# Optimization experiments

Hardware: AMD Instinct MI355X
Metric: run time of the kernel (lower is better)

Reference implementation:

```python
import jax, jax.numpy as jnp
import numpy as np

D_MODEL = 1024
N_HEADS = 16
HEAD_DIM = D_MODEL // N_HEADS
KV_LATENT = 512
N_EXPERTS = 4
D_HIDDEN = 4 * D_MODEL
B, T = 2, 1024


def rmsnorm(x, w, eps=1e-6):
    return w * (x * jax.lax.rsqrt(jnp.mean(x * x, axis=-1, keepdims=True) + eps))


def layernorm(x, g, b, eps=1e-5):
    mu = jnp.mean(x, axis=-1, keepdims=True)
    var = jnp.mean((x - mu) ** 2, axis=-1, keepdims=True)
    return (x - mu) * jax.lax.rsqrt(var + eps) * g + b


def apply_rope(x):
    # x: [b, h, t, d], half-split RoPE as in the torch source
    t, d = x.shape[2], x.shape[3]
    half = d // 2
    pos = jnp.arange(t, dtype=x.dtype)[:, None]                      # [t,1]
    inv_freq = 1.0 / (10000.0 ** (jnp.arange(half, dtype=x.dtype) / half))
    ang = pos * inv_freq[None, :]                                    # [t,half]
    sin, cos = jnp.sin(ang), jnp.cos(ang)
    x1, x2 = x[..., :half], x[..., half:]
    return jnp.concatenate([x1 * cos - x2 * sin, x1 * sin + x2 * cos], axis=-1)


def setup_inputs() -> dict:
    key = jax.random.key(0)
    ks = jax.random.split(key, 16)
    s = lambda fan_in: 1.0 / np.sqrt(fan_in)
    return {
        "x": jax.random.normal(ks[0], (B, T, D_MODEL), jnp.float32),
        "norm1_w": jnp.ones((D_MODEL,), jnp.float32),
        "norm2_w": jnp.ones((D_MODEL,), jnp.float32),
        "Wq": jax.random.normal(ks[1], (D_MODEL, D_MODEL), jnp.float32) * s(D_MODEL),
        "Wdkv": jax.random.normal(ks[2], (KV_LATENT, D_MODEL), jnp.float32) * s(D_MODEL),
        "Wuk": jax.random.normal(ks[3], (D_MODEL, KV_LATENT), jnp.float32) * s(KV_LATENT),
        "Wuv": jax.random.normal(ks[4], (D_MODEL, KV_LATENT), jnp.float32) * s(KV_LATENT),
        "Wo": jax.random.normal(ks[5], (D_MODEL, D_MODEL), jnp.float32) * s(D_MODEL),
        "ln_g": jnp.ones((KV_LATENT,), jnp.float32),
        "ln_b": jnp.zeros((KV_LATENT,), jnp.float32),
        "gate_w": jax.random.normal(ks[6], (N_EXPERTS, D_MODEL), jnp.float32) * s(D_MODEL),
        "gate_b": jnp.zeros((N_EXPERTS,), jnp.float32),
        "W1": jax.random.normal(ks[7], (N_EXPERTS, D_HIDDEN, D_MODEL), jnp.float32) * s(D_MODEL),
        "b1": jnp.zeros((N_EXPERTS, D_HIDDEN), jnp.float32),
        "W2": jax.random.normal(ks[8], (N_EXPERTS, D_MODEL, D_HIDDEN), jnp.float32) * s(D_HIDDEN),
        "b2": jnp.zeros((N_EXPERTS, D_MODEL), jnp.float32),
    }


def mla_attention(x, Wq, Wdkv, Wuk, Wuv, Wo, ln_g, ln_b):
    b, t, _ = x.shape
    q = (x @ Wq.T).reshape(b, t, N_HEADS, HEAD_DIM).transpose(0, 2, 1, 3)  # [b,h,t,dh]
    latent = layernorm(x @ Wdkv.T, ln_g, ln_b)                             # [b,t,L]
    k = (latent @ Wuk.T).reshape(b, t, N_HEADS, HEAD_DIM).transpose(0, 2, 1, 3)
    v = (latent @ Wuv.T).reshape(b, t, N_HEADS, HEAD_DIM).transpose(0, 2, 1, 3)
    q = apply_rope(q)
    k = apply_rope(k)
    scores = jnp.einsum("bhqd,bhkd->bhqk", q, k) / np.sqrt(HEAD_DIM)
    causal = jnp.tril(jnp.ones((t, t), dtype=bool))
    scores = jnp.where(causal, scores, -jnp.inf)
    attn = jax.nn.softmax(scores, axis=-1)  # dropout is identity in eval
    out = jnp.einsum("bhqk,bhkd->bhqd", attn, v).transpose(0, 2, 1, 3).reshape(b, t, D_MODEL)
    return out @ Wo.T


def moe(x, gate_w, gate_b, W1, b1, W2, b2):
    # top-1 routing: each token goes to exactly one expert (argmax of gate)
    logits = x @ gate_w.T + gate_b                                  # [b,t,E]
    top = jnp.argmax(logits, axis=-1)                               # [b,t]
    onehot = jax.nn.one_hot(top, N_EXPERTS, dtype=x.dtype)          # [b,t,E]
    h = jax.nn.relu(jnp.einsum("btd,ehd->bteh", x, W1) + b1)        # [b,t,E,H]
    y = jnp.einsum("bteh,edh->bted", h, W2) + b2                    # [b,t,E,D]
    return jnp.einsum("bted,bte->btd", y, onehot)


def reference(x, norm1_w, norm2_w, Wq, Wdkv, Wuk, Wuv, Wo, ln_g, ln_b,
              gate_w, gate_b, W1, b1, W2, b2):
    x = x + mla_attention(rmsnorm(x, norm1_w), Wq, Wdkv, Wuk, Wuv, Wo, ln_g, ln_b)
    x = x + moe(rmsnorm(x, norm2_w), gate_w, gate_b, W1, b1, W2, b2)
    return x
```

## Files before the change

### kernel.cpp

```cpp
#include <hip/hip_runtime.h>
#include <hip/hip_bf16.h>
#include <math.h>

typedef unsigned short u16;
typedef __attribute__((ext_vector_type(4))) float floatx4;
typedef __attribute__((ext_vector_type(8))) short shortx8;

#define DEVI static __device__ __forceinline__

DEVI u16 f2b(float f) {
  union { float f; unsigned int i; } v; v.f = f;
  unsigned int x = v.i;
  return (u16)((x + 0x7fffu + ((x >> 16) & 1u)) >> 16);
}

constexpr int T_ = 1024, D_ = 1024, HD_ = 64, KV_ = 512, DH_ = 4096, M_ = 2048;
#define NEGBIG (-1e30f)

__global__ __launch_bounds__(256) void k_rms1b(const float* __restrict__ x, const float* __restrict__ w,
                                               u16* __restrict__ outb) {
  int row = blockIdx.x, tid = threadIdx.x;
  float4 v = *(const float4*)&x[(size_t)row * D_ + tid * 4];
  float ss = v.x*v.x + v.y*v.y + v.z*v.z + v.w*v.w;
  #pragma unroll
  for (int m = 32; m >= 1; m >>= 1) ss += __shfl_xor(ss, m, 64);
  __shared__ float red[4];
  if ((tid & 63) == 0) red[tid >> 6] = ss;
  __syncthreads();
  ss = red[0] + red[1] + red[2] + red[3];
  float sc = 1.0f / sqrtf(ss * (1.0f / 1024.0f) + 1e-6f);
  float4 wv = *(const float4*)&w[tid * 4];
  ushort4 ob;
  ob.x = f2b(wv.x*v.x*sc); ob.y = f2b(wv.y*v.y*sc);
  ob.z = f2b(wv.z*v.z*sc); ob.w = f2b(wv.w*v.w*sc);
  *(ushort4*)&outb[(size_t)row * D_ + tid * 4] = ob;
}

__global__ __launch_bounds__(256) void k_rms2b(const float* __restrict__ x, const float* __restrict__ w,
                                               float* __restrict__ outf, u16* __restrict__ outb) {
  int row = blockIdx.x, tid = threadIdx.x;
  float4 v = *(const float4*)&x[(size_t)row * D_ + tid * 4];
  float ss = v.x*v.x + v.y*v.y + v.z*v.z + v.w*v.w;
  #pragma unroll
  for (int m = 32; m >= 1; m >>= 1) ss += __shfl_xor(ss, m, 64);
  __shared__ float red[4];
  if ((tid & 63) == 0) red[tid >> 6] = ss;
  __syncthreads();
  ss = red[0] + red[1] + red[2] + red[3];
  float sc = 1.0f / sqrtf(ss * (1.0f / 1024.0f) + 1e-6f);
  float4 wv = *(const float4*)&w[tid * 4];
  float4 o; o.x = wv.x*v.x*sc; o.y = wv.y*v.y*sc; o.z = wv.z*v.z*sc; o.w = wv.w*v.w*sc;
  *(float4*)&outf[(size_t)row * D_ + tid * 4] = o;
  ushort4 ob; ob.x = f2b(o.x); ob.y = f2b(o.y); ob.z = f2b(o.z); ob.w = f2b(o.w);
  *(ushort4*)&outb[(size_t)row * D_ + tid * 4] = ob;
}

__global__ __launch_bounds__(256) void k_lnb(const float* __restrict__ lat, const float* __restrict__ g,
                                             const float* __restrict__ bb, u16* __restrict__ ob) {
  int row = blockIdx.x, tid = threadIdx.x;
  const float* r = lat + (size_t)row * KV_;
  float v0 = r[tid], v1 = r[tid + 256];
  float s = v0 + v1;
  #pragma unroll
  for (int m = 32; m >= 1; m >>= 1) s += __shfl_xor(s, m, 64);
  __shared__ float red[4];
  if ((tid & 63) == 0) red[tid >> 6] = s;
  __syncthreads();
  float mu = (red[0] + red[1] + red[2] + red[3]) * (1.0f / 512.0f);
  __syncthreads();
  float d0 = v0 - mu, d1 = v1 - mu;
  float ss = d0*d0 + d1*d1;
  #pragma unroll
  for (int m = 32; m >= 1; m >>= 1) ss += __shfl_xor(ss, m, 64);
  if ((tid & 63) == 0) red[tid >> 6] = ss;
  __syncthreads();
  float var = (red[0] + red[1] + red[2] + red[3]) * (1.0f / 512.0f);
  float sc = 1.0f / sqrtf(var + 1e-5f);
  ob[(size_t)row * KV_ + tid]       = f2b(d0 * sc * g[tid]       + bb[tid]);
  ob[(size_t)row * KV_ + tid + 256] = f2b(d1 * sc * g[tid + 256] + bb[tid + 256]);
}

__global__ __launch_bounds__(256) void k_cvtall(const float* __restrict__ W1, const float* __restrict__ W2,
                                                const float* __restrict__ Wq, const float* __restrict__ Wdkv,
                                                const float* __restrict__ Wuk, const float* __restrict__ Wuv,
                                                const float* __restrict__ Wo, u16* __restrict__ dst) {
  for (size_t i = (size_t)blockIdx.x * 256 + threadIdx.x; i < 9306112ull; i += (size_t)gridDim.x * 256) {
    const float* s;
    if      (i < 4194304ull) s = W1   + i * 4;
    else if (i < 8388608ull) s = W2   + (i - 4194304ull) * 4;
    else if (i < 8650752ull) s = Wq   + (i - 8388608ull) * 4;
    else if (i < 8781824ull) s = Wdkv + (i - 8650752ull) * 4;
    else if (i < 8912896ull) s = Wuk  + (i - 8781824ull) * 4;
    else if (i < 9043968ull) s = Wuv  + (i - 8912896ull) * 4;
    else                     s = Wo   + (i - 9043968ull) * 4;
    float4 f = *(const float4*)s;
    ushort4 u; u.x = f2b(f.x); u.y = f2b(f.y); u.z = f2b(f.z); u.w = f2b(f.w);
    *(ushort4*)(dst + i * 4) = u;
  }
}

template<int BF16B>
__global__ __launch_bounds__(256) void k_gemm_t(const u16* __restrict__ A, const void* __restrict__ Bp,
                                                const float* __restrict__ resid, float* __restrict__ Cf,
                                                u16* __restrict__ Cb, int N, int K) {
  int bid = blockIdx.x;
  int xcd = bid & 7, jj = bid >> 3;
  int mt = jj & 31, nt = (jj >> 5) * 8 + xcd;
  __shared__ __align__(16) u16 As[64][72];
  __shared__ __align__(16) u16 Bs[64][72];
  int tid = threadIdx.x, lane = tid & 63, wave = tid >> 6;
  int wm = (wave >> 1) * 32, wn = (wave & 1) * 32;
  int lr = tid >> 2, lc = (tid & 3) * 16;
  const u16* arow = A + (size_t)(mt * 64 + lr) * K + lc;
  const u16* browb = (const u16*)Bp + (size_t)(nt * 64 + lr) * K + lc;
  const float* browf = (const float*)Bp + (size_t)(nt * 64 + lr) * K + lc;
  floatx4 z = {0.f, 0.f, 0.f, 0.f};
  floatx4 acc00 = z, acc01 = z, acc10 = z, acc11 = z;
  int fm = lane & 15, fkq = (lane >> 4) * 8;
  uint4 ra0 = *(const uint4*)&arow[0];
  uint4 ra1 = *(const uint4*)&arow[8];
  uint4 rbA, rbB; float4 rb0, rb1, rb2, rb3;
  if constexpr (BF16B) {
    rbA = *(const uint4*)&browb[0]; rbB = *(const uint4*)&browb[8];
  } else {
    rb0 = *(const float4*)&browf[0];  rb1 = *(const float4*)&browf[4];
    rb2 = *(const float4*)&browf[8];  rb3 = *(const float4*)&browf[12];
  }
  for (int kb = 0; kb < K; kb += 64) {
    *(uint4*)&As[lr][lc]     = ra0;
    *(uint4*)&As[lr][lc + 8] = ra1;
    if constexpr (BF16B) {
      *(uint4*)&Bs[lr][lc]     = rbA;
      *(uint4*)&Bs[lr][lc + 8] = rbB;
    } else {
      ushort4 u;
      u.x = f2b(rb0.x); u.y = f2b(rb0.y); u.z = f2b(rb0.z); u.w = f2b(rb0.w); *(ushort4*)&Bs[lr][lc]      = u;
      u.x = f2b(rb1.x); u.y = f2b(rb1.y); u.z = f2b(rb1.z); u.w = f2b(rb1.w); *(ushort4*)&Bs[lr][lc + 4]  = u;
      u.x = f2b(rb2.x); u.y = f2b(rb2.y); u.z = f2b(rb2.z); u.w = f2b(rb2.w); *(ushort4*)&Bs[lr][lc + 8]  = u;
      u.x = f2b(rb3.x); u.y = f2b(rb3.y); u.z = f2b(rb3.z); u.w = f2b(rb3.w); *(ushort4*)&Bs[lr][lc + 12] = u;
    }
    __syncthreads();
    if (kb + 64 < K) {
      ra0 = *(const uint4*)&arow[kb + 64];
      ra1 = *(const uint4*)&arow[kb + 72];
      if constexpr (BF16B) {
        rbA = *(const uint4*)&browb[kb + 64]; rbB = *(const uint4*)&browb[kb + 72];
      } else {
        rb0 = *(const float4*)&browf[kb + 64]; rb1 = *(const float4*)&browf[kb + 68];
        rb2 = *(const float4*)&browf[kb + 72]; rb3 = *(const float4*)&browf[kb + 76];
      }
    }
    #pragma unroll
    for (int ks = 0; ks < 64; ks += 32) {
      shortx8 a0  = *(const shortx8*)&As[wm + fm][ks + fkq];
      shortx8 a1  = *(const shortx8*)&As[wm + 16 + fm][ks + fkq];
      shortx8 b0  = *(const shortx8*)&Bs[wn + fm][ks + fkq];
      shortx8 b1v = *(const shortx8*)&Bs[wn + 16 + fm][ks + fkq];
      acc00 = __builtin_amdgcn_mfma_f32_16x16x32_bf16(a0, b0,  acc00, 0, 0, 0);
      acc01 = __builtin_amdgcn_mfma_f32_16x16x32_bf16(a0, b1v, acc01, 0, 0, 0);
      acc10 = __builtin_amdgcn_mfma_f32_16x16x32_bf16(a1, b0,  acc10, 0, 0, 0);
      acc11 = __builtin_amdgcn_mfma_f32_16x16x32_bf16(a1, b1v, acc11, 0, 0, 0);
    }
    __syncthreads();
  }
  int q4 = (lane >> 4) * 4, cix = lane & 15;
  #pragma unroll
  for (int im = 0; im < 2; ++im) {
    #pragma unroll
    for (int rg = 0; rg < 4; ++rg) {
      int row = mt * 64 + wm + im * 16 + q4 + rg;
      #pragma unroll
      for (int in = 0; in < 2; ++in) {
        int gn = nt * 64 + wn + in * 16 + cix;
        float vv = (im == 0 ? (in == 0 ? acc00[rg] : acc01[rg]) : (in == 0 ? acc10[rg] : acc11[rg]));
        size_t idx = (size_t)row * N + gn;
        if (Cb) {
          Cb[idx] = f2b(vv);
        } else {
          if (resid) vv += resid[idx];
          Cf[idx] = vv;
        }
      }
    }
  }
}

__global__ __launch_bounds__(256) void k_rope2b(const float* __restrict__ q, const float* __restrict__ k,
                                                u16* __restrict__ qb, u16* __restrict__ kb) {
  int g = blockIdx.x * 256 + threadIdx.x;
  int j = g & 31;
  int h = (g >> 5) & 15;
  int row = g >> 9;
  int t = row & (T_ - 1);
  float p = (float)pow(10000.0, (double)j * (1.0 / 32.0));
  float ang = (float)t / p;
  float sn, cs; sincosf(ang, &sn, &cs);
  size_t base = (size_t)row * D_ + h * 64 + j;
  float x1 = q[base], x2 = q[base + 32];
  qb[base]      = f2b((x1 * cs - x2 * sn) * 0.125f);
  qb[base + 32] = f2b((x1 * sn + x2 * cs) * 0.125f);
  x1 = k[base]; x2 = k[base + 32];
  kb[base]      = f2b(x1 * cs - x2 * sn);
  kb[base + 32] = f2b(x1 * sn + x2 * cs);
}

__global__ __launch_bounds__(256) void k_fattn(const u16* __restrict__ qbp, const u16* __restrict__ kbp,
                                               const u16* __restrict__ vbp, u16* __restrict__ ob) {
  int idx = blockIdx.x, h = blockIdx.y;
  int b = idx >> 4;
  int qt = idx & 15;
  if (b) qt = 15 - qt;
  __shared__ __align__(16) u16 Qs[64][72];
  __shared__ __align__(16) u16 Ks[64][72];
  __shared__ __align__(16) u16 Vs[64][72];
  __shared__ __align__(16) u16 Ps[64][72];
  __shared__ float red1[2][64];
  __shared__ float red2[2][64];
  int tid = threadIdx.x, lane = tid & 63, wave = tid >> 6;
  int wm = (wave >> 1) * 32, wn = (wave & 1) * 32, w1 = wave & 1;
  int fm = lane & 15, fkq = (lane >> 4) * 8;
  int q4 = (lane >> 4) * 4, cix = lane & 15;
  size_t rowbase = (size_t)b * T_;
  int colbase = h * HD_;
  int q0 = qt * 64;
  int lr = tid >> 2, ld = (tid & 3) * 16;
  {
    const u16* qr = qbp + (rowbase + q0 + lr) * D_ + colbase + ld;
    *(uint4*)&Qs[lr][ld]     = *(const uint4*)&qr[0];
    *(uint4*)&Qs[lr][ld + 8] = *(const uint4*)&qr[8];
  }
  floatx4 z = {0.f, 0.f, 0.f, 0.f};
  floatx4 s[2][2], o[2][2];
  o[0][0] = z; o[0][1] = z; o[1][0] = z; o[1][1] = z;
  float m[2][4], l[2][4], f_[2][4];
  #pragma unroll
  for (int im = 0; im < 2; ++im)
    #pragma unroll
    for (int rg = 0; rg < 4; ++rg) { m[im][rg] = NEGBIG; l[im][rg] = 0.f; }
  for (int kt = 0; kt <= qt; ++kt) {
    __syncthreads();
    {
      const u16* kr = kbp + (rowbase + kt * 64 + lr) * D_ + colbase + ld;
      *(uint4*)&Ks[lr][ld]     = *(const uint4*)&kr[0];
      *(uint4*)&Ks[lr][ld + 8] = *(const uint4*)&kr[8];
      const u16* vr = vbp + (rowbase + kt * 64 + lr) * D_ + colbase + ld;
      #pragma unroll
      for (int c = 0; c < 16; ++c) Vs[ld + c][lr] = vr[c];
    }
    __syncthreads();
    s[0][0] = z; s[0][1] = z; s[1][0] = z; s[1][1] = z;
    #pragma unroll
    for (int ks = 0; ks < 64; ks += 32) {
      shortx8 a0  = *(const shortx8*)&Qs[wm + fm][ks + fkq];
      shortx8 a1  = *(const shortx8*)&Qs[wm + 16 + fm][ks + fkq];
      shortx8 b0  = *(const shortx8*)&Ks[wn + fm][ks + fkq];
      shortx8 b1v = *(const shortx8*)&Ks[wn + 16 + fm][ks + fkq];
      s[0][0] = __builtin_amdgcn_mfma_f32_16x16x32_bf16(a0, b0,  s[0][0], 0, 0, 0);
      s[0][1] = __builtin_amdgcn_mfma_f32_16x16x32_bf16(a0, b1v, s[0][1], 0, 0, 0);
      s[1][0] = __builtin_amdgcn_mfma_f32_16x16x32_bf16(a1, b0,  s[1][0], 0, 0, 0);
      s[1][1] = __builtin_amdgcn_mfma_f32_16x16x32_bf16(a1, b1v, s[1][1], 0, 0, 0);
    }
    if (kt == qt) {
      #pragma unroll
      for (int im = 0; im < 2; ++im)
        #pragma unroll
        for (int rg = 0; rg < 4; ++rg) {
          int r = wm + im * 16 + q4 + rg;
          #pragma unroll
          for (int in = 0; in < 2; ++in)
            if (wn + in * 16 + cix > r) s[im][in][rg] = NEGBIG;
        }
    }
    #pragma unroll
    for (int im = 0; im < 2; ++im)
      #pragma unroll
      for (int rg = 0; rg < 4; ++rg) {
        float pm = fmaxf(s[im][0][rg], s[im][1][rg]);
        #pragma unroll
        for (int mk = 8; mk >= 1; mk >>= 1) pm = fmaxf(pm, __shfl_xor(pm, mk, 64));
        if (cix == 0) red1[w1][wm + im * 16 + q4 + rg] = pm;
        f_[im][rg] = pm;
      }
    __syncthreads();
    #pragma unroll
    for (int im = 0; im < 2; ++im)
      #pragma unroll
      for (int rg = 0; rg < 4; ++rg) {
        int r = wm + im * 16 + q4 + rg;
        float mx = fmaxf(f_[im][rg], red1[w1 ^ 1][r]);
        float mn = fmaxf(m[im][rg], mx);
        float f = __expf(m[im][rg] - mn);
        m[im][rg] = mn;
        float p0 = __expf(s[im][0][rg] - mn);
        float p1 = __expf(s[im][1][rg] - mn);
        float ss = p0 + p1;
        #pragma unroll
        for (int mk = 8; mk >= 1; mk >>= 1) ss += __shfl_xor(ss, mk, 64);
        if (cix == 0) red2[w1][r] = ss;
        Ps[r][wn + cix]      = f2b(p0);
        Ps[r][wn + 16 + cix] = f2b(p1);
        l[im][rg] *= f;
        o[im][0][rg] *= f;
        o[im][1][rg] *= f;
      }
    __syncthreads();
    #pragma unroll
    for (int im = 0; im < 2; ++im)
      #pragma unroll
      for (int rg = 0; rg < 4; ++rg) {
        int r = wm + im * 16 + q4 + rg;
        l[im][rg] += red2[0][r] + red2[1][r];
      }
    #pragma unroll
    for (int ks = 0; ks < 64; ks += 32) {
      shortx8 a0  = *(const shortx8*)&Ps[wm + fm][ks + fkq];
      shortx8 a1  = *(const shortx8*)&Ps[wm + 16 + fm][ks + fkq];
      shortx8 b0  = *(const shortx8*)&Vs[wn + fm][ks + fkq];
      shortx8 b1v = *(const shortx8*)&Vs[wn + 16 + fm][ks + fkq];
      o[0][0] = __builtin_amdgcn_mfma_f32_16x16x32_bf16(a0, b0,  o[0][0], 0, 0, 0);
      o[0][1] = __builtin_amdgcn_mfma_f32_16x16x32_bf16(a0, b1v, o[0][1], 0, 0, 0);
      o[1][0] = __builtin_amdgcn_mfma_f32_16x16x32_bf16(a1, b0,  o[1][0], 0, 0, 0);
      o[1][1] = __builtin_amdgcn_mfma_f32_16x16x32_bf16(a1, b1v, o[1][1], 0, 0, 0);
    }
  }
  #pragma unroll
  for (int im = 0; im < 2; ++im)
    #pragma unroll
    for (int rg = 0; rg < 4; ++rg) {
      int r = wm + im * 16 + q4 + rg;
      float inv = 1.0f / l[im][rg];
      size_t base = (rowbase + q0 + r) * D_ + colbase;
      ob[base + wn + cix]      = f2b(o[im][0][rg] * inv);
      ob[base + wn + 16 + cix] = f2b(o[im][1][rg] * inv);
    }
}

__global__ __launch_bounds__(256) void k_init(int* cnt) { if (threadIdx.x < 4) cnt[threadIdx.x] = 0; }

__global__ __launch_bounds__(256) void k_gate(const float* __restrict__ h2, const float* __restrict__ gw,
                                              const float* __restrict__ gb, int* __restrict__ expert,
                                              int* __restrict__ cnt) {
  int wid = threadIdx.x >> 6, lane = threadIdx.x & 63;
  int t = blockIdx.x * 4 + wid;
  const float* hr = h2 + (size_t)t * D_;
  float a0 = 0, a1 = 0, a2 = 0, a3 = 0;
  for (int c = lane; c < D_; c += 64) {
    float xv = hr[c];
    a0 += xv * gw[c];
    a1 += xv * gw[D_ + c];
    a2 += xv * gw[2 * D_ + c];
    a3 += xv * gw[3 * D_ + c];
  }
  #pragma unroll
  for (int m = 32; m >= 1; m >>= 1) {
    a0 += __shfl_xor(a0, m, 64); a1 += __shfl_xor(a1, m, 64);
    a2 += __shfl_xor(a2, m, 64); a3 += __shfl_xor(a3, m, 64);
  }
  if (lane == 0) {
    float l0 = a0 + gb[0], l1 = a1 + gb[1], l2 = a2 + gb[2], l3 = a3 + gb[3];
    int best = 0; float bv = l0;
    if (l1 > bv) { bv = l1; best = 1; }
    if (l2 > bv) { bv = l2; best = 2; }
    if (l3 > bv) { bv = l3; best = 3; }
    expert[t] = best;
    atomicAdd(&cnt[best], 1);
  }
}

__global__ __launch_bounds__(256) void k_scatter(const int* __restrict__ expert, const int* __restrict__ cnt,
                                                 int* __restrict__ off, int* __restrict__ sorted) {
  __shared__ int cur[4];
  if (threadIdx.x == 0) {
    int o0 = 0, o1 = cnt[0], o2 = o1 + cnt[1], o3 = o2 + cnt[2];
    off[0] = o0; off[1] = o1; off[2] = o2; off[3] = o3;
    cur[0] = o0; cur[1] = o1; cur[2] = o2; cur[3] = o3;
  }
  __syncthreads();
  for (int t = threadIdx.x; t < M_; t += 256) {
    int e = expert[t];
    int p = atomicAdd(&cur[e], 1);
    sorted[p] = t;
  }
}

template<int BF16B>
__global__ __launch_bounds__(256) void k_moe1_t(const u16* __restrict__ A, const void* __restrict__ W1p,
                                                const float* __restrict__ b1, const int* __restrict__ cnt,
                                                const int* __restrict__ off, const int* __restrict__ sorted,
                                                u16* __restrict__ hbuf) {
  int bid = blockIdx.x;
  int xcd = bid & 7, jj = bid >> 3;
  int mt = jj & 31, combo = (jj >> 5) * 8 + xcd;
  int e = combo >> 6, nt = combo & 63;
  int rem = cnt[e] - mt * 64;
  if (rem <= 0) return;
  __shared__ __align__(16) u16 As[64][72];
  __shared__ __align__(16) u16 Bs[64][72];
  int tid = threadIdx.x, lane = tid & 63, wave = tid >> 6;
  int wm = (wave >> 1) * 32, wn = (wave & 1) * 32;
  int lr = tid >> 2, lc = (tid & 3) * 16;
  int rr = lr < rem ? lr : rem - 1;
  const u16* arow = A + (size_t)sorted[off[e] + mt * 64 + rr] * D_ + lc;
  const u16* browb = (const u16*)W1p + (size_t)e * DH_ * D_ + (size_t)(nt * 64 + lr) * D_ + lc;
  const float* browf = (const float*)W1p + (size_t)e * DH_ * D_ + (size_t)(nt * 64 + lr) * D_ + lc;
  floatx4 z = {0.f, 0.f, 0.f, 0.f};
  floatx4 acc00 = z, acc01 = z, acc10 = z, acc11 = z;
  int fm = lane & 15, fkq = (lane >> 4) * 8;
  uint4 ra0 = *(const uint4*)&arow[0];
  uint4 ra1 = *(const uint4*)&arow[8];
  uint4 rbA, rbB; float4 rb0, rb1, rb2, rb3;
  if constexpr (BF16B) {
    rbA = *(const uint4*)&browb[0]; rbB = *(const uint4*)&browb[8];
  } else {
    rb0 = *(const float4*)&browf[0];  rb1 = *(const float4*)&browf[4];
    rb2 = *(const float4*)&browf[8];  rb3 = *(const float4*)&browf[12];
  }
  for (int kb = 0; kb < D_; kb += 64) {
    *(uint4*)&As[lr][lc]     = ra0;
    *(uint4*)&As[lr][lc + 8] = ra1;
    if constexpr (BF16B) {
      *(uint4*)&Bs[lr][lc]     = rbA;
      *(uint4*)&Bs[lr][lc + 8] = rbB;
    } else {
      ushort4 u;
      u.x = f2b(rb0.x); u.y = f2b(rb0.y); u.z = f2b(rb0.z); u.w = f2b(rb0.w); *(ushort4*)&Bs[lr][lc]      = u;
      u.x = f2b(rb1.x); u.y = f2b(rb1.y); u.z = f2b(rb1.z); u.w = f2b(rb1.w); *(ushort4*)&Bs[lr][lc + 4]  = u;
      u.x = f2b(rb2.x); u.y = f2b(rb2.y); u.z = f2b(rb2.z); u.w = f2b(rb2.w); *(ushort4*)&Bs[lr][lc + 8]  = u;
      u.x = f2b(rb3.x); u.y = f2b(rb3.y); u.z = f2b(rb3.z); u.w = f2b(rb3.w); *(ushort4*)&Bs[lr][lc + 12] = u;
    }
    __syncthreads();
    if (kb + 64 < D_) {
      ra0 = *(const uint4*)&arow[kb + 64];
      ra1 = *(const uint4*)&arow[kb + 72];
      if constexpr (BF16B) {
        rbA = *(const uint4*)&browb[kb + 64]; rbB = *(const uint4*)&browb[kb + 72];
      } else {
        rb0 = *(const float4*)&browf[kb + 64]; rb1 = *(const float4*)&browf[kb + 68];
        rb2 = *(const float4*)&browf[kb + 72]; rb3 = *(const float4*)&browf[kb + 76];
      }
    }
    #pragma unroll
    for (int ks = 0; ks < 64; ks += 32) {
      shortx8 a0  = *(const shortx8*)&As[wm + fm][ks + fkq];
      shortx8 a1  = *(const shortx8*)&As[wm + 16 + fm][ks + fkq];
      shortx8 b0  = *(const shortx8*)&Bs[wn + fm][ks + fkq];
      shortx8 b1v = *(const shortx8*)&Bs[wn + 16 + fm][ks + fkq];
      acc00 = __builtin_amdgcn_mfma_f32_16x16x32_bf16(a0, b0,  acc00, 0, 0, 0);
      acc01 = __builtin_amdgcn_mfma_f32_16x16x32_bf16(a0, b1v, acc01, 0, 0, 0);
      acc10 = __builtin_amdgcn_mfma_f32_16x16x32_bf16(a1, b0,  acc10, 0, 0, 0);
      acc11 = __builtin_amdgcn_mfma_f32_16x16x32_bf16(a1, b1v, acc11, 0, 0, 0);
    }
    __syncthreads();
  }
  int q4 = (lane >> 4) * 4, cix = lane & 15;
  #pragma unroll
  for (int im = 0; im < 2; ++im) {
    #pragma unroll
    for (int rg = 0; rg < 4; ++rg) {
      int ml = wm + im * 16 + q4 + rg;
      if (ml >= rem) continue;
      size_t grow = (size_t)(off[e] + mt * 64 + ml);
      #pragma unroll
      for (int in = 0; in < 2; ++in) {
        int gn = nt * 64 + wn + in * 16 + cix;
        float vv = (im == 0 ? (in == 0 ? acc00[rg] : acc01[rg]) : (in == 0 ? acc10[rg] : acc11[rg]));
        vv += b1[e * DH_ + gn];
        hbuf[grow * DH_ + gn] = f2b(fmaxf(vv, 0.f));
      }
    }
  }
}

template<int BF16B>
__global__ __launch_bounds__(256) void k_moe2_t(const u16* __restrict__ hbuf, const void* __restrict__ W2p,
                                                const float* __restrict__ b2w, const float* __restrict__ x1f,
                                                const int* __restrict__ cnt, const int* __restrict__ off,
                                                const int* __restrict__ sorted, float* __restrict__ out) {
  int bid = blockIdx.x;
  int xcd = bid & 7, jj = bid >> 3;
  int mt = jj & 31, combo = (jj >> 5) * 8 + xcd;
  int e = combo >> 4, nt = combo & 15;
  int rem = cnt[e] - mt * 64;
  if (rem <= 0) return;
  __shared__ __align__(16) u16 As[64][72];
  __shared__ __align__(16) u16 Bs[64][72];
  int tid = threadIdx.x, lane = tid & 63, wave = tid >> 6;
  int wm = (wave >> 1) * 32, wn = (wave & 1) * 32;
  int lr = tid >> 2, lc = (tid & 3) * 16;
  int rr = lr < rem ? lr : rem - 1;
  const u16* arow = hbuf + (size_t)(off[e] + mt * 64 + rr) * DH_ + lc;
  const u16* browb = (const u16*)W2p + (size_t)e * D_ * DH_ + (size_t)(nt * 64 + lr) * DH_ + lc;
  const float* browf = (const float*)W2p + (size_t)e * D_ * DH_ + (size_t)(nt * 64 + lr) * DH_ + lc;
  floatx4 z = {0.f, 0.f, 0.f, 0.f};
  floatx4 acc00 = z, acc01 = z, acc10 = z, acc11 = z;
  int fm = lane & 15, fkq = (lane >> 4) * 8;
  uint4 ra0 = *(const uint4*)&arow[0];
  uint4 ra1 = *(const uint4*)&arow[8];
  uint4 rbA, rbB; float4 rb0, rb1, rb2, rb3;
  if constexpr (BF16B) {
    rbA = *(const uint4*)&browb[0]; rbB = *(const uint4*)&browb[8];
  } else {
    rb0 = *(const float4*)&browf[0];  rb1 = *(const float4*)&browf[4];
    rb2 = *(const float4*)&browf[8];  rb3 = *(const float4*)&browf[12];
  }
  for (int kb = 0; kb < DH_; kb += 64) {
    *(uint4*)&As[lr][lc]     = ra0;
    *(uint4*)&As[lr][lc + 8] = ra1;
    if constexpr (BF16B) {
      *(uint4*)&Bs[lr][lc]     = rbA;
      *(uint4*)&Bs[lr][lc + 8] = rbB;
    } else {
      ushort4 u;
      u.x = f2b(rb0.x); u.y = f2b(rb0.y); u.z = f2b(rb0.z); u.w = f2b(rb0.w); *(ushort4*)&Bs[lr][lc]      = u;
      u.x = f2b(rb1.x); u.y = f2b(rb1.y); u.z = f2b(rb1.z); u.w = f2b(rb1.w); *(ushort4*)&Bs[lr][lc + 4]  = u;
      u.x = f2b(rb2.x); u.y = f2b(rb2.y); u.z = f2b(rb2.z); u.w = f2b(rb2.w); *(ushort4*)&Bs[lr][lc + 8]  = u;
      u.x = f2b(rb3.x); u.y = f2b(rb3.y); u.z = f2b(rb3.z); u.w = f2b(rb3.w); *(ushort4*)&Bs[lr][lc + 12] = u;
    }
    __syncthreads();
    if (kb + 64 < DH_) {
      ra0 = *(const uint4*)&arow[kb + 64];
      ra1 = *(const uint4*)&arow[kb + 72];
      if constexpr (BF16B) {
        rbA = *(const uint4*)&browb[kb + 64]; rbB = *(const uint4*)&browb[kb + 72];
      } else {
        rb0 = *(const float4*)&browf[kb + 64]; rb1 = *(const float4*)&browf[kb + 68];
        rb2 = *(const float4*)&browf[kb + 72]; rb3 = *(const float4*)&browf[kb + 76];
      }
    }
    #pragma unroll
    for (int ks = 0; ks < 64; ks += 32) {
      shortx8 a0  = *(const shortx8*)&As[wm + fm][ks + fkq];
      shortx8 a1  = *(const shortx8*)&As[wm + 16 + fm][ks + fkq];
      shortx8 b0  = *(const shortx8*)&Bs[wn + fm][ks + fkq];
      shortx8 b1v = *(const shortx8*)&Bs[wn + 16 + fm][ks + fkq];
      acc00 = __builtin_amdgcn_mfma_f32_16x16x32_bf16(a0, b0,  acc00, 0, 0, 0);
      acc01 = __builtin_amdgcn_mfma_f32_16x16x32_bf16(a0, b1v, acc01, 0, 0, 0);
      acc10 = __builtin_amdgcn_mfma_f32_16x16x32_bf16(a1, b0,  acc10, 0, 0, 0);
      acc11 = __builtin_amdgcn_mfma_f32_16x16x32_bf16(a1, b1v, acc11, 0, 0, 0);
    }
    __syncthreads();
  }
  int q4 = (lane >> 4) * 4, cix = lane & 15;
  #pragma unroll
  for (int im = 0; im < 2; ++im) {
    #pragma unroll
    for (int rg = 0; rg < 4; ++rg) {
      int ml = wm + im * 16 + q4 + rg;
      if (ml >= rem) continue;
      int tok = sorted[off[e] + mt * 64 + ml];
      #pragma unroll
      for (int in = 0; in < 2; ++in) {
        int gn = nt * 64 + wn + in * 16 + cix;
        float vv = (im == 0 ? (in == 0 ? acc00[rg] : acc01[rg]) : (in == 0 ? acc10[rg] : acc11[rg]));
        out[(size_t)tok * D_ + gn] = vv + b2w[e * D_ + gn] + x1f[(size_t)tok * D_ + gn];
      }
    }
  }
}

extern "C" void kernel_launch(void* const* d_in, const int* in_sizes, int n_in,
                              void* d_out, int out_size, void* d_ws, size_t ws_size,
                              hipStream_t stream) {
  int map[16];
  for (int i = 0; i < 16; ++i) map[i] = i;
  if (n_in == 16 && in_sizes[0] == 16777216) {
    const int mm[16] = {15, 13, 14, 4, 2, 5, 6, 3, 12, 11, 10, 9, 0, 7, 1, 8};
    for (int i = 0; i < 16; ++i) map[i] = mm[i];
  } else if (n_in == 16 && in_sizes[0] == 4096) {
    for (int i = 0; i < 16; ++i) map[i] = 15 - i;
  }
  const float* x    = (const float*)d_in[map[0]];
  const float* n1w  = (const float*)d_in[map[1]];
  const float* n2w  = (const float*)d_in[map[2]];
  const float* Wq   = (const float*)d_in[map[3]];
  const float* Wdkv = (const float*)d_in[map[4]];
  const float* Wuk  = (const float*)d_in[map[5]];
  const float* Wuv  = (const float*)d_in[map[6]];
  const float* Wo   = (const float*)d_in[map[7]];
  const float* lng  = (const float*)d_in[map[8]];
  const float* lnb  = (const float*)d_in[map[9]];
  const float* gw   = (const float*)d_in[map[10]];
  const float* gb   = (const float*)d_in[map[11]];
  const float* W1   = (const float*)d_in[map[12]];
  const float* b1   = (const float*)d_in[map[13]];
  const float* W2   = (const float*)d_in[map[14]];
  const float* b2w  = (const float*)d_in[map[15]];
  float* out = (float*)d_out;
  char* ws = (char*)d_ws;
  const size_t MB = 1ull << 20;
  float* qf   = (float*)(ws + 0);
  float* x1f  = (float*)(ws + 0);
  float* kf   = (float*)(ws + 8 * MB);
  u16*   hbuf = (u16*)(ws + 8 * MB);
  float* latf = (float*)(ws + 16 * MB);
  u16*   qb   = (u16*)(ws + 16 * MB);
  u16*   h1b  = (u16*)(ws + 20 * MB);
  u16*   kb   = (u16*)(ws + 20 * MB);
  u16*   latb = (u16*)(ws + 24 * MB);
  float* h2f  = (float*)(ws + 24 * MB);
  u16*   vb   = (u16*)(ws + 26 * MB);
  u16*   ab   = (u16*)(ws + 30 * MB);
  u16*   h2b  = (u16*)(ws + 32 * MB);

  bool big = ws_size >= (107ull * MB + (64ull << 10));
  u16* wb = (u16*)(ws + 36 * MB);
  u16* W1b   = wb;
  u16* W2b   = wb + 16777216;
  u16* Wqb   = wb + 33554432;
  u16* Wdkvb = wb + 34603008;
  u16* Wukb  = wb + 35127296;
  u16* Wuvb  = wb + 35651584;
  u16* Wob   = wb + 36175872;
  int* cnt    = (int*)(ws + (big ? 107 * MB : 36 * MB));
  int* off    = cnt + 8;
  int* expert = cnt + 16;
  int* sorted = expert + 2048;

  if (big) {
    k_cvtall<<<2048, 256, 0, stream>>>(W1, W2, Wq, Wdkv, Wuk, Wuv, Wo, wb);
    k_rms1b<<<2048, 256, 0, stream>>>(x, n1w, h1b);
    k_gemm_t<1><<<512, 256, 0, stream>>>(h1b, Wqb, nullptr, qf, nullptr, 1024, 1024);
    k_gemm_t<1><<<256, 256, 0, stream>>>(h1b, Wdkvb, nullptr, latf, nullptr, 512, 1024);
    k_lnb<<<2048, 256, 0, stream>>>(latf, lng, lnb, latb);
    k_gemm_t<1><<<512, 256, 0, stream>>>(latb, Wukb, nullptr, kf, nullptr, 1024, 512);
    k_gemm_t<1><<<512, 256, 0, stream>>>(latb, Wuvb, nullptr, nullptr, vb, 1024, 512);
    k_rope2b<<<4096, 256, 0, stream>>>(qf, kf, qb, kb);
    k_fattn<<<dim3(32, 16), 256, 0, stream>>>(qb, kb, vb, ab);
    k_gemm_t<1><<<512, 256, 0, stream>>>(ab, Wob, x, x1f, nullptr, 1024, 1024);
    k_rms2b<<<2048, 256, 0, stream>>>(x1f, n2w, h2f, h2b);
    k_init<<<1, 64, 0, stream>>>(cnt);
    k_gate<<<512, 256, 0, stream>>>(h2f, gw, gb, expert, cnt);
    k_scatter<<<1, 256, 0, stream>>>(expert, cnt, off, sorted);
    k_moe1_t<1><<<8192, 256, 0, stream>>>(h2b, W1b, b1, cnt, off, sorted, hbuf);
    k_moe2_t<1><<<2048, 256, 0, stream>>>(hbuf, W2b, b2w, x1f, cnt, off, sorted, out);
  } else {
    k_rms1b<<<2048, 256, 0, stream>>>(x, n1w, h1b);
    k_gemm_t<0><<<512, 256, 0, stream>>>(h1b, Wq, nullptr, qf, nullptr, 1024, 1024);
    k_gemm_t<0><<<256, 256, 0, stream>>>(h1b, Wdkv, nullptr, latf, nullptr, 512, 1024);
    k_lnb<<<2048, 256, 0, stream>>>(latf, lng, lnb, latb);
    k_gemm_t<0><<<512, 256, 0, stream>>>(latb, Wuk, nullptr, kf, nullptr, 1024, 512);
    k_gemm_t<0><<<512, 256, 0, stream>>>(latb, Wuv, nullptr, nullptr, vb, 1024, 512);
    k_rope2b<<<4096, 256, 0, stream>>>(qf, kf, qb, kb);
    k_fattn<<<dim3(32, 16), 256, 0, stream>>>(qb, kb, vb, ab);
    k_gemm_t<0><<<512, 256, 0, stream>>>(ab, Wo, x, x1f, nullptr, 1024, 1024);
    k_rms2b<<<2048, 256, 0, stream>>>(x1f, n2w, h2f, h2b);
    k_init<<<1, 64, 0, stream>>>(cnt);
    k_gate<<<512, 256, 0, stream>>>(h2f, gw, gb, expert, cnt);
    k_scatter<<<1, 256, 0, stream>>>(expert, cnt, off, sorted);
    k_moe1_t<0><<<8192, 256, 0, stream>>>(h2b, W1, b1, cnt, off, sorted, hbuf);
    k_moe2_t<0><<<2048, 256, 0, stream>>>(hbuf, W2, b2w, x1f, cnt, off, sorted, out);
  }
}
```

Baseline: 501.1 us.

## Split MoE down-projection GEMM along K with a separate reduction kernel

Splits the second MoE GEMM (hidden 4096 down to 1024) into two K-halves, so twice as many blocks write fp32 partial sums to a workspace buffer. A new per-token reduction kernel adds both partials, the expert bias and the residual, then scatters the result to the output. The aim is more active blocks per CU, since top-1 routing leaves most of the original grid idle after early exits. The cost is an extra kernel launch and about 16MB of fp32 partials written and read back. The partial buffer also overlaps the converted-weight region, which is safe only because those weights are regenerated every call.

```diff
diff --git a/kernel.cpp b/kernel.cpp
--- a/kernel.cpp
+++ b/kernel.cpp
@@ -556,6 +556,97 @@
       }
     }
   }
+}
+
+__global__ __launch_bounds__(256) void k_moe2s(const u16* __restrict__ hbuf, const u16* __restrict__ W2b,
+                                               const int* __restrict__ cnt, const int* __restrict__ off,
+                                               float* __restrict__ pbuf) {
+  int bid = blockIdx.x;
+  int xcd = bid & 7, jj = bid >> 3;
+  int mt = jj & 31;
+  int combo = (jj >> 5) * 8 + xcd;
+  int ks = combo & 1, ec = combo >> 1;
+  int e = ec >> 4, nt = ec & 15;
+  int rem = cnt[e] - mt * 64;
+  if (rem <= 0) return;
+  const int KS = DH_ / 2;
+  int k0 = ks * KS;
+  __shared__ __align__(16) u16 As[64][72];
+  __shared__ __align__(16) u16 Bs[64][72];
+  int tid = threadIdx.x, lane = tid & 63, wave = tid >> 6;
+  int wm = (wave >> 1) * 32, wn = (wave & 1) * 32;
+  int lr = tid >> 2, lc = (tid & 3) * 16;
+  int rr = lr < rem ? lr : rem - 1;
+  const u16* arow = hbuf + (size_t)(off[e] + mt * 64 + rr) * DH_ + k0 + lc;
+  const u16* brow = W2b + (size_t)e * D_ * DH_ + (size_t)(nt * 64 + lr) * DH_ + k0 + lc;
+  floatx4 z = {0.f, 0.f, 0.f, 0.f};
+  floatx4 acc00 = z, acc01 = z, acc10 = z, acc11 = z;
+  int fm = lane & 15, fkq = (lane >> 4) * 8;
+  uint4 ra0 = *(const uint4*)&arow[0];
+  uint4 ra1 = *(const uint4*)&arow[8];
+  uint4 rbA = *(const uint4*)&brow[0];
+  uint4 rbB = *(const uint4*)&brow[8];
+  for (int kb = 0; kb < KS; kb += 64) {
+    *(uint4*)&As[lr][lc]     = ra0;
+    *(uint4*)&As[lr][lc + 8] = ra1;
+    *(uint4*)&Bs[lr][lc]     = rbA;
+    *(uint4*)&Bs[lr][lc + 8] = rbB;
+    __syncthreads();
+    if (kb + 64 < KS) {
+      ra0 = *(const uint4*)&arow[kb + 64];
+      ra1 = *(const uint4*)&arow[kb + 72];
+      rbA = *(const uint4*)&brow[kb + 64];
+      rbB = *(const uint4*)&brow[kb + 72];
+    }
+    #pragma unroll
+    for (int kk = 0; kk < 64; kk += 32) {
+      shortx8 a0  = *(const shortx8*)&As[wm + fm][kk + fkq];
+      shortx8 a1  = *(const shortx8*)&As[wm + 16 + fm][kk + fkq];
+      shortx8 b0  = *(const shortx8*)&Bs[wn + fm][kk + fkq];
+      shortx8 b1v = *(const shortx8*)&Bs[wn + 16 + fm][kk + fkq];
+      acc00 = __builtin_amdgcn_mfma_f32_16x16x32_bf16(a0, b0,  acc00, 0, 0, 0);
+      acc01 = __builtin_amdgcn_mfma_f32_16x16x32_bf16(a0, b1v, acc01, 0, 0, 0);
+      acc10 = __builtin_amdgcn_mfma_f32_16x16x32_bf16(a1, b0,  acc10, 0, 0, 0);
+      acc11 = __builtin_amdgcn_mfma_f32_16x16x32_bf16(a1, b1v, acc11, 0, 0, 0);
+    }
+    __syncthreads();
+  }
+  float* pb = pbuf + (size_t)ks * M_ * D_;
+  int q4 = (lane >> 4) * 4, cix = lane & 15;
+  #pragma unroll
+  for (int im = 0; im < 2; ++im) {
+    #pragma unroll
+    for (int rg = 0; rg < 4; ++rg) {
+      int ml = wm + im * 16 + q4 + rg;
+      if (ml >= rem) continue;
+      size_t srow = (size_t)(off[e] + mt * 64 + ml);
+      #pragma unroll
+      for (int in = 0; in < 2; ++in) {
+        int gn = nt * 64 + wn + in * 16 + cix;
+        float vv = (im == 0 ? (in == 0 ? acc00[rg] : acc01[rg]) : (in == 0 ? acc10[rg] : acc11[rg]));
+        pb[srow * D_ + gn] = vv;
+      }
+    }
+  }
+}
+
+__global__ __launch_bounds__(256) void k_moered(const float* __restrict__ pbuf, const float* __restrict__ b2w,
+                                                const float* __restrict__ x1f, const int* __restrict__ off,
+                                                const int* __restrict__ sorted, float* __restrict__ out) {
+  int r = blockIdx.x, tid = threadIdx.x;
+  int tok = sorted[r];
+  int e = (r >= off[3]) ? 3 : (r >= off[2]) ? 2 : (r >= off[1]) ? 1 : 0;
+  size_t c = (size_t)tid * 4;
+  float4 a = *(const float4*)&pbuf[(size_t)r * D_ + c];
+  float4 b = *(const float4*)&pbuf[(size_t)M_ * D_ + (size_t)r * D_ + c];
+  float4 bb = *(const float4*)&b2w[(size_t)e * D_ + c];
+  float4 xr = *(const float4*)&x1f[(size_t)tok * D_ + c];
+  float4 o;
+  o.x = a.x + b.x + bb.x + xr.x;
+  o.y = a.y + b.y + bb.y + xr.y;
+  o.z = a.z + b.z + bb.z + xr.z;
+  o.w = a.w + b.w + bb.w + xr.w;
+  *(float4*)&out[(size_t)tok * D_ + c] = o;
 }
 
 extern "C" void kernel_launch(void* const* d_in, const int* in_sizes, int n_in,
@@ -601,6 +692,7 @@
   u16*   vb   = (u16*)(ws + 26 * MB);
   u16*   ab   = (u16*)(ws + 30 * MB);
   u16*   h2b  = (u16*)(ws + 32 * MB);
+  float* pbuf = (float*)(ws + 24 * MB);
 
   bool big = ws_size >= (107ull * MB + (64ull << 10));
   u16* wb = (u16*)(ws + 36 * MB);
@@ -632,7 +724,8 @@
     k_gate<<<512, 256, 0, stream>>>(h2f, gw, gb, expert, cnt);
     k_scatter<<<1, 256, 0, stream>>>(expert, cnt, off, sorted);
     k_moe1_t<1><<<8192, 256, 0, stream>>>(h2b, W1b, b1, cnt, off, sorted, hbuf);
-    k_moe2_t<1><<<2048, 256, 0, stream>>>(hbuf, W2b, b2w, x1f, cnt, off, sorted, out);
+    k_moe2s<<<4096, 256, 0, stream>>>(hbuf, W2b, cnt, off, pbuf);
+    k_moered<<<2048, 256, 0, stream>>>(pbuf, b2w, x1f, off, sorted, out);
   } else {
     k_rms1b<<<2048, 256, 0, stream>>>(x, n1w, h1b);
     k_gemm_t<0><<<512, 256, 0, stream>>>(h1b, Wq, nullptr, qf, nullptr, 1024, 1024);
```

Result: faster. 468.7 us (-6.5%).
